# Optimization experiments

Measured on AMD Instinct MI355X. Metric: run time of the kernel, lower is better.

Reference implementation:

```python
import jax, jax.numpy as jnp
import numpy as np

PEAK_W = 2.0
HIGH_W = 1.0
OVERALL_W = 0.5
HIGH_RATIO = 0.8
NEG = -1e30  # sentinel for masked max (avoids -inf -> nan in grads)


def setup_inputs() -> dict:
    key = jax.random.key(0)
    k1, k2, k3 = jax.random.split(key, 3)
    B, S = 2048, 8192
    predictions = jax.random.normal(k1, (B, S, 1), dtype=jnp.float32)
    targets = jax.random.normal(k2, (B, S, 1), dtype=jnp.float32)
    flood_mask = jax.random.randint(k3, (B, S, 1), 0, 2, dtype=jnp.int32)
    return {"predictions": predictions, "targets": targets, "flood_mask": flood_mask}


def _safe_rmse(sum_sq, n):
    # sqrt(mean) with zero-count guard that is safe under autodiff
    nz = n > 0
    ms = sum_sq / jnp.maximum(n, 1).astype(sum_sq.dtype)
    return jnp.where(nz, jnp.sqrt(jnp.where(nz, ms, 1.0)), 0.0)


def reference(predictions, targets, flood_mask):
    p = predictions[:, :, 0]            # [B, S]
    t = targets[:, :, 0]                # [B, S]
    m = flood_mask[:, :, 0].astype(bool)
    valid = m & ~jnp.isnan(p) & ~jnp.isnan(t)          # flood & finite
    n = valid.sum(axis=1)                               # [B]
    nz = n > 0

    sq = jnp.where(valid, (p - t) ** 2, 0.0)
    overall_rmse = _safe_rmse(sq.sum(axis=1), n)

    t_peak = jnp.max(jnp.where(valid, t, NEG), axis=1)  # [B]
    p_peak = jnp.max(jnp.where(valid, p, NEG), axis=1)
    peak_error = jnp.where(nz, jnp.abs(p_peak - t_peak), 0.0)

    # high-value region: targ >= target_peak * high_ratio (all valid if peak <= 0)
    thr = t_peak * HIGH_RATIO
    high = valid & jnp.where((t_peak <= 0)[:, None], True, t >= thr[:, None])
    nh = high.sum(axis=1)
    high_rmse = _safe_rmse(jnp.where(high, (p - t) ** 2, 0.0).sum(axis=1), nh)

    loss = OVERALL_W * overall_rmse + PEAK_W * peak_error + HIGH_W * high_rmse  # [B]
    return jnp.mean(loss)  # reduction='mean'
```

## Files before the change

### kernel.cpp

```cpp
#include <hip/hip_runtime.h>
#include <math.h>


#define S_LEN 8192
#define BLK   1024
#define NWAVE (BLK / 64)
#define VEC   (S_LEN / 4 / BLK)

__device__ __forceinline__ float waveSum(float x) {
    #pragma unroll
    for (int o = 32; o > 0; o >>= 1) x += __shfl_down(x, o, 64);
    return x;
}
__device__ __forceinline__ float waveMax(float x) {
    #pragma unroll
    for (int o = 32; o > 0; o >>= 1) x = fmaxf(x, __shfl_down(x, o, 64));
    return x;
}

__global__ __launch_bounds__(BLK) void flood_loss_kernel(
    const float* __restrict__ P, const float* __restrict__ T,
    const int* __restrict__ M, float* __restrict__ out, float invB)
{
    __shared__ float red[NWAVE][4];

    const int tid  = threadIdx.x;
    const int wid  = tid >> 6;
    const int lane = tid & 63;
    const size_t base = (size_t)blockIdx.x * S_LEN;

    const float4* __restrict__ P4 = (const float4*)(P + base);
    const float4* __restrict__ T4 = (const float4*)(T + base);
    const int4*   __restrict__ M4 = (const int4*)(M + base);

    float tenc[VEC * 4];
    float d2v [VEC * 4];
    float ssq = 0.f, fn = 0.f;
    float tpk = -INFINITY, ppk = -INFINITY;

    #pragma unroll
    for (int it = 0; it < VEC; ++it) {
        const int v = it * BLK + tid;
        float4 p4 = P4[v];
        float4 t4 = T4[v];
        int4   m4 = M4[v];
        float pe[4] = {p4.x, p4.y, p4.z, p4.w};
        float te[4] = {t4.x, t4.y, t4.z, t4.w};
        int   me[4] = {m4.x, m4.y, m4.z, m4.w};
        #pragma unroll
        for (int j = 0; j < 4; ++j) {
            bool valid = (me[j] != 0) && !(pe[j] != pe[j]) && !(te[j] != te[j]);
            float d  = pe[j] - te[j];
            float d2 = valid ? d * d : 0.f;
            ssq += d2;
            fn  += valid ? 1.f : 0.f;
            if (valid) { tpk = fmaxf(tpk, te[j]); ppk = fmaxf(ppk, pe[j]); }
            tenc[it * 4 + j] = valid ? te[j] : -INFINITY;
            d2v [it * 4 + j] = d2;
        }
        asm volatile("" : "+v"(tenc[it*4+0]), "+v"(tenc[it*4+1]),
                          "+v"(tenc[it*4+2]), "+v"(tenc[it*4+3]),
                          "+v"(d2v [it*4+0]), "+v"(d2v [it*4+1]),
                          "+v"(d2v [it*4+2]), "+v"(d2v [it*4+3]));
    }

    ssq = waveSum(ssq); fn = waveSum(fn);
    tpk = waveMax(tpk); ppk = waveMax(ppk);
    if (lane == 0) { red[wid][0] = fn; red[wid][1] = ssq; red[wid][2] = tpk; red[wid][3] = ppk; }
    __syncthreads();

    float fnT = 0.f, ssqT = 0.f, tpkT = -INFINITY, ppkT = -INFINITY;
    #pragma unroll
    for (int w = 0; w < NWAVE; ++w) {
        fnT  += red[w][0];
        ssqT += red[w][1];
        tpkT  = fmaxf(tpkT, red[w][2]);
        ppkT  = fmaxf(ppkT, red[w][3]);
    }

    const bool  tpos = tpkT > 0.f;
    const float thr  = tpkT * 0.8f;
    float nh = 0.f, ssqh = 0.f;
    #pragma unroll
    for (int k = 0; k < VEC * 4; ++k) {
        bool hi = tpos ? (tenc[k] >= thr) : (tenc[k] > -INFINITY);
        nh   += hi ? 1.f : 0.f;
        ssqh += hi ? d2v[k] : 0.f;
    }
    nh = waveSum(nh); ssqh = waveSum(ssqh);
    __syncthreads();
    if (lane == 0) { red[wid][0] = nh; red[wid][1] = ssqh; }
    __syncthreads();

    if (tid == 0) {
        float nht = 0.f, ssqht = 0.f;
        #pragma unroll
        for (int w = 0; w < NWAVE; ++w) { nht += red[w][0]; ssqht += red[w][1]; }
        float overall = (fnT > 0.f) ? sqrtf(ssqT  / fmaxf(fnT, 1.f)) : 0.f;
        float high_r  = (nht > 0.f) ? sqrtf(ssqht / fmaxf(nht, 1.f)) : 0.f;
        float peak_e  = (fnT > 0.f) ? fabsf(ppkT - tpkT) : 0.f;
        float loss = 0.5f * overall + 2.0f * peak_e + 1.0f * high_r;
        atomicAdd(out, loss * invB);
    }
}

extern "C" void kernel_launch(void* const* d_in, const int* in_sizes, int n_in,
                              void* d_out, int out_size, void* d_ws, size_t ws_size,
                              hipStream_t stream) {
    const float* P = (const float*)d_in[0];
    const float* T = (const float*)d_in[1];
    const int*   M = (const int*)d_in[2];
    float* out = (float*)d_out;
    const int B = in_sizes[0] / S_LEN;

    hipMemsetAsync(out, 0, sizeof(float), stream);
    flood_loss_kernel<<<B, BLK, 0, stream>>>(P, T, M, out, 1.0f / (float)B);
}
```

Baseline: 197.0 us.

## Process four rows per block and replace atomics with a two-stage reduction

Each block now loops over four rows instead of one, so the grid has a quarter as many blocks. Every block writes its summed loss to a workspace slot, and a second single-block kernel sums those slots. This removes the memset and the 2048 same-address atomicAdds. The cost is fewer blocks in flight and a serial row loop per block, which may leave less memory-level parallelism on a bandwidth-bound kernel. The reduce kernel assumes NBLK <= 512.

Result: slower. 203.2 us (+3.1%).

```diff
diff --git a/kernel.cpp b/kernel.cpp
--- a/kernel.cpp
+++ b/kernel.cpp
@@ -6,6 +6,7 @@
 #define BLK   1024
 #define NWAVE (BLK / 64)
 #define VEC   (S_LEN / 4 / BLK)
+#define ROWS_PER_BLK 4
 
 __device__ __forceinline__ float waveSum(float x) {
     #pragma unroll
@@ -18,89 +19,115 @@
     return x;
 }
 
-__global__ __launch_bounds__(BLK) void flood_loss_kernel(
+__global__ __launch_bounds__(BLK) void flood_loss_rows(
     const float* __restrict__ P, const float* __restrict__ T,
-    const int* __restrict__ M, float* __restrict__ out, float invB)
+    const int* __restrict__ M, float* __restrict__ partial)
 {
     __shared__ float red[NWAVE][4];
 
     const int tid  = threadIdx.x;
     const int wid  = tid >> 6;
     const int lane = tid & 63;
-    const size_t base = (size_t)blockIdx.x * S_LEN;
 
-    const float4* __restrict__ P4 = (const float4*)(P + base);
-    const float4* __restrict__ T4 = (const float4*)(T + base);
-    const int4*   __restrict__ M4 = (const int4*)(M + base);
+    float losssum = 0.f;
 
-    float tenc[VEC * 4];
-    float d2v [VEC * 4];
-    float ssq = 0.f, fn = 0.f;
-    float tpk = -INFINITY, ppk = -INFINITY;
+    for (int r = 0; r < ROWS_PER_BLK; ++r) {
+        const size_t row  = (size_t)blockIdx.x * ROWS_PER_BLK + r;
+        const size_t base = row * S_LEN;
+        const float4* __restrict__ P4 = (const float4*)(P + base);
+        const float4* __restrict__ T4 = (const float4*)(T + base);
+        const int4*   __restrict__ M4 = (const int4*)(M + base);
 
-    #pragma unroll
-    for (int it = 0; it < VEC; ++it) {
-        const int v = it * BLK + tid;
-        float4 p4 = P4[v];
-        float4 t4 = T4[v];
-        int4   m4 = M4[v];
-        float pe[4] = {p4.x, p4.y, p4.z, p4.w};
-        float te[4] = {t4.x, t4.y, t4.z, t4.w};
-        int   me[4] = {m4.x, m4.y, m4.z, m4.w};
+        float tenc[VEC * 4];
+        float d2v [VEC * 4];
+        float ssq = 0.f, fn = 0.f;
+        float tpk = -INFINITY, ppk = -INFINITY;
+
         #pragma unroll
-        for (int j = 0; j < 4; ++j) {
-            bool valid = (me[j] != 0) && !(pe[j] != pe[j]) && !(te[j] != te[j]);
-            float d  = pe[j] - te[j];
-            float d2 = valid ? d * d : 0.f;
-            ssq += d2;
-            fn  += valid ? 1.f : 0.f;
-            if (valid) { tpk = fmaxf(tpk, te[j]); ppk = fmaxf(ppk, pe[j]); }
-            tenc[it * 4 + j] = valid ? te[j] : -INFINITY;
-            d2v [it * 4 + j] = d2;
+        for (int it = 0; it < VEC; ++it) {
+            const int v = it * BLK + tid;
+            float4 p4 = P4[v];
+            float4 t4 = T4[v];
+            int4   m4 = M4[v];
+            float pe[4] = {p4.x, p4.y, p4.z, p4.w};
+            float te[4] = {t4.x, t4.y, t4.z, t4.w};
+            int   me[4] = {m4.x, m4.y, m4.z, m4.w};
+            #pragma unroll
+            for (int j = 0; j < 4; ++j) {
+                bool valid = (me[j] != 0) && !(pe[j] != pe[j]) && !(te[j] != te[j]);
+                float d  = pe[j] - te[j];
+                float d2 = valid ? d * d : 0.f;
+                ssq += d2;
+                fn  += valid ? 1.f : 0.f;
+                if (valid) { tpk = fmaxf(tpk, te[j]); ppk = fmaxf(ppk, pe[j]); }
+                tenc[it * 4 + j] = valid ? te[j] : -INFINITY;
+                d2v [it * 4 + j] = d2;
+            }
+            asm volatile("" : "+v"(tenc[it*4+0]), "+v"(tenc[it*4+1]),
+                              "+v"(tenc[it*4+2]), "+v"(tenc[it*4+3]),
+                              "+v"(d2v [it*4+0]), "+v"(d2v [it*4+1]),
+                              "+v"(d2v [it*4+2]), "+v"(d2v [it*4+3]));
         }
-        asm volatile("" : "+v"(tenc[it*4+0]), "+v"(tenc[it*4+1]),
-                          "+v"(tenc[it*4+2]), "+v"(tenc[it*4+3]),
-                          "+v"(d2v [it*4+0]), "+v"(d2v [it*4+1]),
-                          "+v"(d2v [it*4+2]), "+v"(d2v [it*4+3]));
+
+        ssq = waveSum(ssq); fn = waveSum(fn);
+        tpk = waveMax(tpk); ppk = waveMax(ppk);
+        if (lane == 0) { red[wid][0] = fn; red[wid][1] = ssq; red[wid][2] = tpk; red[wid][3] = ppk; }
+        __syncthreads();
+
+        float fnT = 0.f, ssqT = 0.f, tpkT = -INFINITY, ppkT = -INFINITY;
+        #pragma unroll
+        for (int w = 0; w < NWAVE; ++w) {
+            fnT  += red[w][0];
+            ssqT += red[w][1];
+            tpkT  = fmaxf(tpkT, red[w][2]);
+            ppkT  = fmaxf(ppkT, red[w][3]);
+        }
+
+        const bool  tpos = tpkT > 0.f;
+        const float thr  = tpkT * 0.8f;
+        float nh = 0.f, ssqh = 0.f;
+        #pragma unroll
+        for (int k = 0; k < VEC * 4; ++k) {
+            bool hi = tpos ? (tenc[k] >= thr) : (tenc[k] > -INFINITY);
+            nh   += hi ? 1.f : 0.f;
+            ssqh += hi ? d2v[k] : 0.f;
+        }
+        nh = waveSum(nh); ssqh = waveSum(ssqh);
+        __syncthreads();
+        if (lane == 0) { red[wid][0] = nh; red[wid][1] = ssqh; }
+        __syncthreads();
+
+        if (tid == 0) {
+            float nht = 0.f, ssqht = 0.f;
+            #pragma unroll
+            for (int w = 0; w < NWAVE; ++w) { nht += red[w][0]; ssqht += red[w][1]; }
+            float overall = (fnT > 0.f) ? sqrtf(ssqT  / fmaxf(fnT, 1.f)) : 0.f;
+            float high_r  = (nht > 0.f) ? sqrtf(ssqht / fmaxf(nht, 1.f)) : 0.f;
+            float peak_e  = (fnT > 0.f) ? fabsf(ppkT - tpkT) : 0.f;
+            losssum += 0.5f * overall + 2.0f * peak_e + 1.0f * high_r;
+        }
+        __syncthreads();
     }
 
-    ssq = waveSum(ssq); fn = waveSum(fn);
-    tpk = waveMax(tpk); ppk = waveMax(ppk);
-    if (lane == 0) { red[wid][0] = fn; red[wid][1] = ssq; red[wid][2] = tpk; red[wid][3] = ppk; }
+    if (tid == 0) partial[blockIdx.x] = losssum;
+}
+
+__global__ __launch_bounds__(512) void flood_loss_reduce(
+    const float* __restrict__ partial, float* __restrict__ out, float invB, int n)
+{
+    __shared__ float s[8];
+    const int tid  = threadIdx.x;
+    const int wid  = tid >> 6;
+    const int lane = tid & 63;
+    float x = (tid < n) ? partial[tid] : 0.f;
+    x = waveSum(x);
+    if (lane == 0) s[wid] = x;
     __syncthreads();
-
-    float fnT = 0.f, ssqT = 0.f, tpkT = -INFINITY, ppkT = -INFINITY;
-    #pragma unroll
-    for (int w = 0; w < NWAVE; ++w) {
-        fnT  += red[w][0];
-        ssqT += red[w][1];
-        tpkT  = fmaxf(tpkT, red[w][2]);
-        ppkT  = fmaxf(ppkT, red[w][3]);
-    }
-
-    const bool  tpos = tpkT > 0.f;
-    const float thr  = tpkT * 0.8f;
-    float nh = 0.f, ssqh = 0.f;
-    #pragma unroll
-    for (int k = 0; k < VEC * 4; ++k) {
-        bool hi = tpos ? (tenc[k] >= thr) : (tenc[k] > -INFINITY);
-        nh   += hi ? 1.f : 0.f;
-        ssqh += hi ? d2v[k] : 0.f;
-    }
-    nh = waveSum(nh); ssqh = waveSum(ssqh);
-    __syncthreads();
-    if (lane == 0) { red[wid][0] = nh; red[wid][1] = ssqh; }
-    __syncthreads();
-
     if (tid == 0) {
-        float nht = 0.f, ssqht = 0.f;
+        float tot = 0.f;
         #pragma unroll
-        for (int w = 0; w < NWAVE; ++w) { nht += red[w][0]; ssqht += red[w][1]; }
-        float overall = (fnT > 0.f) ? sqrtf(ssqT  / fmaxf(fnT, 1.f)) : 0.f;
-        float high_r  = (nht > 0.f) ? sqrtf(ssqht / fmaxf(nht, 1.f)) : 0.f;
-        float peak_e  = (fnT > 0.f) ? fabsf(ppkT - tpkT) : 0.f;
-        float loss = 0.5f * overall + 2.0f * peak_e + 1.0f * high_r;
-        atomicAdd(out, loss * invB);
+        for (int w = 0; w < 8; ++w) tot += s[w];
+        out[0] = tot * invB;
     }
 }
 
@@ -111,8 +138,10 @@
     const float* T = (const float*)d_in[1];
     const int*   M = (const int*)d_in[2];
     float* out = (float*)d_out;
-    const int B = in_sizes[0] / S_LEN;
+    float* partial = (float*)d_ws;
+    const int B    = in_sizes[0] / S_LEN;
+    const int NBLK = B / ROWS_PER_BLK;
 
-    hipMemsetAsync(out, 0, sizeof(float), stream);
-    flood_loss_kernel<<<B, BLK, 0, stream>>>(P, T, M, out, 1.0f / (float)B);
+    flood_loss_rows<<<NBLK, BLK, 0, stream>>>(P, T, M, partial);
+    flood_loss_reduce<<<1, 512, 0, stream>>>(partial, out, 1.0f / (float)B, NBLK);
 }
```
